# Performance work log

Measured on AMD Instinct MI355X. Metric: run time of the kernel, lower is better.

## Reference

```python
import jax, jax.numpy as jnp
import numpy as np

WS = 8        # window_size
SHIFT = 4     # shift_size
NH = 6        # num_heads
EPS = 1e-5


def _rel_pos_index(ws):
    coords = np.stack(np.meshgrid(np.arange(ws), np.arange(ws), indexing='ij'))  # [2,ws,ws]
    cf = coords.reshape(2, -1)                      # [2, ws*ws]
    rel = cf[:, :, None] - cf[:, None, :]           # [2, N, N]
    rel = rel.transpose(1, 2, 0)                    # [N, N, 2]
    rel[:, :, 0] += ws - 1
    rel[:, :, 1] += ws - 1
    rel[:, :, 0] *= 2 * ws - 1
    return rel.sum(-1)                              # [N, N] int


def _attn_mask(H, W, ws, shift):
    img = np.zeros((H, W), dtype=np.float32)
    slices = (slice(0, -ws), slice(-ws, -shift), slice(-shift, None))
    cnt = 0
    for hs in slices:
        for wsl in slices:
            img[hs, wsl] = cnt
            cnt += 1
    mw = img.reshape(H // ws, ws, W // ws, ws).transpose(0, 2, 1, 3).reshape(-1, ws * ws)
    diff = mw[:, None, :] - mw[:, :, None]          # [nW, N, N]
    return np.where(diff != 0, -100.0, 0.0).astype(np.float32)


def _layernorm(x, g, b):
    mu = x.mean(-1, keepdims=True)
    var = ((x - mu) ** 2).mean(-1, keepdims=True)
    return (x - mu) * jax.lax.rsqrt(var + EPS) * g + b


def setup_inputs() -> dict:
    key = jax.random.key(0)
    ks = jax.random.split(key, 8)
    C, HID = 192, 768
    return {
        'x': jax.random.normal(ks[0], (8, 128, 128, C), jnp.float32),
        'g1': jnp.ones((C,), jnp.float32),
        'b1': jnp.zeros((C,), jnp.float32),
        'qkv_w': jax.random.normal(ks[1], (3 * C, C), jnp.float32) * 0.02,
        'qkv_b': jnp.zeros((3 * C,), jnp.float32),
        'rpb_table': jax.random.normal(ks[2], ((2 * WS - 1) ** 2, NH), jnp.float32) * 0.02,
        'proj_w': jax.random.normal(ks[3], (C, C), jnp.float32) * 0.02,
        'proj_b': jnp.zeros((C,), jnp.float32),
        'g2': jnp.ones((C,), jnp.float32),
        'b2': jnp.zeros((C,), jnp.float32),
        'fc1_w': jax.random.normal(ks[4], (HID, C), jnp.float32) * 0.02,
        'fc1_b': jnp.zeros((HID,), jnp.float32),
        'fc2_w': jax.random.normal(ks[5], (C, HID), jnp.float32) * 0.02,
        'fc2_b': jnp.zeros((C,), jnp.float32),
    }


def reference(x, g1, b1, qkv_w, qkv_b, rpb_table, proj_w, proj_b, g2, b2,
              fc1_w, fc1_b, fc2_w, fc2_b):
    B, H, W, C = x.shape
    N = WS * WS
    hd = C // NH
    scale = hd ** -0.5

    rpi = jnp.asarray(_rel_pos_index(WS))                 # [N,N] static
    mask = jnp.asarray(_attn_mask(H, W, WS, SHIFT))       # [nW,N,N] static
    nW = mask.shape[0]

    shortcut = x.reshape(B, H * W, C)
    xn = _layernorm(shortcut, g1, b1).reshape(B, H, W, C)

    # cyclic shift
    xs = jnp.roll(xn, shift=(-SHIFT, -SHIFT), axis=(1, 2))

    # window partition -> [B*nW, N, C]
    win = xs.reshape(B, H // WS, WS, W // WS, WS, C).transpose(0, 1, 3, 2, 4, 5)
    win = win.reshape(-1, N, C)
    B_ = win.shape[0]

    # qkv
    qkv = jnp.einsum('bnc,oc->bno', win, qkv_w) + qkv_b   # [B_,N,3C]
    qkv = qkv.reshape(B_, N, 3, NH, hd).transpose(2, 0, 3, 1, 4)  # [3,B_,NH,N,hd]
    q, k, v = qkv[0] * scale, qkv[1], qkv[2]

    attn = jnp.einsum('bhnd,bhmd->bhnm', q, k)            # [B_,NH,N,N]
    bias = rpb_table[rpi.reshape(-1)].reshape(N, N, NH).transpose(2, 0, 1)
    attn = attn + bias[None]
    attn = attn.reshape(B, nW, NH, N, N) + mask[None, :, None]
    attn = jax.nn.softmax(attn.reshape(B_, NH, N, N), axis=-1)

    out = jnp.einsum('bhnm,bhmd->bhnd', attn, v)          # [B_,NH,N,hd]
    out = out.transpose(0, 2, 1, 3).reshape(B_, N, C)
    out = jnp.einsum('bnc,oc->bno', out, proj_w) + proj_b

    # window reverse -> [B,H,W,C]
    out = out.reshape(B, H // WS, W // WS, WS, WS, C).transpose(0, 1, 3, 2, 4, 5)
    out = out.reshape(B, H, W, C)
    out = jnp.roll(out, shift=(SHIFT, SHIFT), axis=(1, 2)).reshape(B, H * W, C)

    x1 = shortcut + out
    h = _layernorm(x1, g2, b2)
    h = jnp.einsum('bnc,hc->bnh', h, fc1_w) + fc1_b
    h = jax.nn.gelu(h, approximate=False)
    h = jnp.einsum('bnh,ch->bnc', h, fc2_w) + fc2_b
    x2 = x1 + h
    return x2.reshape(B, H, W, C)
```

## Files before the change

kernel.cpp:

```cpp
#include <hip/hip_runtime.h>
#include <hip/hip_bf16.h>

typedef __attribute__((ext_vector_type(8))) short s16x8;
typedef __attribute__((ext_vector_type(4))) float f32x4;

__device__ __forceinline__ unsigned short f2bf(float f){
    __hip_bfloat16 h = __float2bfloat16(f);
    return *reinterpret_cast<unsigned short*>(&h);
}

__device__ __forceinline__ int flab(int g){ return (g < 120) ? 0 : ((g < 124) ? 1 : 2); }

__device__ __forceinline__ void async16(const void* g, void* l){
    __builtin_amdgcn_global_load_lds(
        (const __attribute__((address_space(1))) unsigned int*)g,
        (__attribute__((address_space(3))) unsigned int*)l, 16, 0, 0);
}

__global__ __launch_bounds__(256) void wconv_all(
    const float* __restrict__ w0, const float* __restrict__ w1,
    const float* __restrict__ w2, const float* __restrict__ w3,
    unsigned short* __restrict__ o0, unsigned short* __restrict__ o1,
    unsigned short* __restrict__ o2, unsigned short* __restrict__ o3)
{
    int i = blockIdx.x*256 + threadIdx.x;
    if (i < 110592) o0[i] = f2bf(w0[i]);
    if (i < 36864)  o1[i] = f2bf(w1[i]);
    if (i < 147456) o2[i] = f2bf(w2[i]);
    if (i < 147456) o3[i] = f2bf(w3[i]);
}

__global__ __launch_bounds__(256) void lnqkv_kernel(
    const float* __restrict__ x, const float* __restrict__ g1, const float* __restrict__ b1,
    const unsigned short* __restrict__ wq, const float* __restrict__ qkvb,
    unsigned short* __restrict__ qo, unsigned short* __restrict__ ko,
    unsigned short* __restrict__ vo)
{
    __shared__ __attribute__((aligned(16))) unsigned short win[64*200];
    __shared__ __attribute__((aligned(16))) unsigned short Bs[64*200];
    const int b_ = blockIdx.x;
    const int bb = b_>>8, wi = b_&255, wh = wi>>4, ww = wi&15;
    const int tid = threadIdx.x;
    const int wv = tid>>6, lane = tid&63, lrow = lane&15, quad = lane>>4;

    {
        const int n = tid>>2, q4 = tid&3;
        const int r = n>>3, c = n&7;
        const int hh = (wh*8 + r + 4)&127, wp = (ww*8 + c + 4)&127;
        const float* px = x + (((size_t)bb*128+hh)*128+wp)*192 + q4*48;
        float v[48];
        #pragma unroll
        for (int m=0;m<12;++m) *(float4*)(v+m*4) = *(const float4*)(px+m*4);
        float s = 0.f;
        #pragma unroll
        for (int k=0;k<48;++k) s += v[k];
        s += __shfl_xor(s,1); s += __shfl_xor(s,2);
        float mu = s*(1.0f/192.0f);
        float qv = 0.f;
        #pragma unroll
        for (int k=0;k<48;++k){ float d=v[k]-mu; qv += d*d; }
        qv += __shfl_xor(qv,1); qv += __shfl_xor(qv,2);
        float rstd = rsqrtf(qv*(1.0f/192.0f) + 1e-5f);
        const float* pg = g1 + q4*48;
        const float* pb = b1 + q4*48;
        unsigned short* pw = win + n*200 + q4*48;
        #pragma unroll
        for (int k=0;k<48;++k) pw[k] = f2bf((v[k]-mu)*rstd*pg[k] + pb[k]);
    }
    __syncthreads();

    s16x8 af[6];
    #pragma unroll
    for (int kc=0;kc<6;++kc)
        af[kc] = *(const s16x8*)(win + (wv*16+lrow)*200 + kc*32 + quad*8);

    for (int ot=0; ot<9; ++ot) {
        const int o0 = ot*64;
        __syncthreads();
        #pragma unroll
        for (int t=0;t<6;++t) {
            int cid = tid + t*256;
            *(int4*)(Bs + (cid/24)*200 + (cid%24)*8) =
                *(const int4*)(wq + (size_t)o0*192 + cid*8);
        }
        __syncthreads();
        f32x4 acc[4];
        #pragma unroll
        for (int j=0;j<4;++j) acc[j] = (f32x4){0.f,0.f,0.f,0.f};
        #pragma unroll
        for (int kc=0;kc<6;++kc)
            #pragma unroll
            for (int j=0;j<4;++j) {
                s16x8 bf = *(const s16x8*)(Bs + (j*16+lrow)*200 + kc*32 + quad*8);
                acc[j] = __builtin_amdgcn_mfma_f32_16x16x32_bf16(af[kc], bf, acc[j], 0, 0, 0);
            }
        __syncthreads();
        unsigned short* T = Bs;
        const int part = ot/3;
        float bv[4];
        #pragma unroll
        for (int j=0;j<4;++j) bv[j] = qkvb[o0 + j*16 + lrow];

        if (part < 2) {
            const float scale = (part==0) ? 0.17677669529663687f : 1.0f;
            #pragma unroll
            for (int j=0;j<4;++j)
                #pragma unroll
                for (int rg=0;rg<4;++rg) {
                    int n2 = wv*16 + quad*4 + rg;
                    T[n2*72 + j*16 + lrow] = f2bf((acc[j][rg]+bv[j])*scale);
                }
            __syncthreads();
            unsigned short* dst = (part==0) ? qo : ko;
            #pragma unroll
            for (int t=0;t<2;++t) {
                int c = tid + t*256;
                int n2 = c>>3, blk = c&7;
                int o_in = o0 + blk*8 - part*192;
                int head = o_in>>5, d = o_in&31;
                *(int4*)(dst + (((size_t)b_*6+head)*64 + n2)*32 + d) =
                    *(const int4*)(T + n2*72 + blk*8);
            }
        } else {
            #pragma unroll
            for (int j=0;j<4;++j)
                #pragma unroll
                for (int rg=0;rg<4;++rg) {
                    int n2 = wv*16 + quad*4 + rg;
                    T[(j*16+lrow)*72 + n2] = f2bf(acc[j][rg]+bv[j]);
                }
            __syncthreads();
            #pragma unroll
            for (int t=0;t<2;++t) {
                int c = tid + t*256;
                int ol = c>>3, nb = (c&7)*8;
                int o_in = o0 + ol - 384;
                int head = o_in>>5, d = o_in&31;
                *(int4*)(vo + (((size_t)b_*6+head)*32 + d)*64 + nb) =
                    *(const int4*)(T + ol*72 + nb);
            }
        }
    }
}

__global__ __launch_bounds__(384) void attn_kernel(
    const unsigned short* __restrict__ q, const unsigned short* __restrict__ k,
    const unsigned short* __restrict__ vT, const float* __restrict__ rpb,
    unsigned short* __restrict__ ao)
{
    __shared__ float rpb_s[1350];
    __shared__ __attribute__((aligned(16))) unsigned short p_lds[6*4608];
    const int b_ = blockIdx.x;
    const int h = threadIdx.x >> 6;
    const int lane = threadIdx.x & 63, lrow = lane & 15, quad = lane >> 4;
    for (int i = threadIdx.x; i < 1350; i += 384) rpb_s[i] = rpb[i];
    __syncthreads();

    const size_t hb = ((size_t)b_*6 + h)*2048;
    const unsigned short* qb = q  + hb;
    const unsigned short* kb = k  + hb;
    const unsigned short* vb = vT + hb;

    s16x8 qf[4], kf[4];
    #pragma unroll
    for (int i = 0; i < 4; ++i) qf[i] = *(const s16x8*)(qb + (i*16+lrow)*32 + quad*8);
    #pragma unroll
    for (int j = 0; j < 4; ++j) kf[j] = *(const s16x8*)(kb + (j*16+lrow)*32 + quad*8);

    const f32x4 zz = {0.f,0.f,0.f,0.f};
    f32x4 s[4][4];
    #pragma unroll
    for (int i = 0; i < 4; ++i)
        #pragma unroll
        for (int j = 0; j < 4; ++j)
            s[i][j] = __builtin_amdgcn_mfma_f32_16x16x32_bf16(qf[i], kf[j], zz, 0, 0, 0);

    const int wi = b_ & 255, wh = wi >> 4, ww = wi & 15;
    int labm[4];
    #pragma unroll
    for (int j = 0; j < 4; ++j) {
        int m = j*16 + lrow;
        labm[j] = flab(wh*8 + (m >> 3))*3 + flab(ww*8 + (m & 7));
    }
    unsigned short* pl = p_lds + h*4608;
    #pragma unroll
    for (int i = 0; i < 4; ++i) {
        #pragma unroll
        for (int rg = 0; rg < 4; ++rg) {
            int n = i*16 + quad*4 + rg;
            int rn = n >> 3, cn = n & 7;
            int labn = flab(wh*8 + rn)*3 + flab(ww*8 + cn);
            float vals[4];
            float vmax = -1e30f;
            #pragma unroll
            for (int j = 0; j < 4; ++j) {
                int m = j*16 + lrow;
                int idx = ((rn - (m >> 3) + 7)*15 + (cn - (m & 7) + 7))*6 + h;
                float val = s[i][j][rg] + rpb_s[idx];
                if (labn != labm[j]) val -= 100.f;
                vals[j] = val;
                vmax = fmaxf(vmax, val);
            }
            #pragma unroll
            for (int o = 1; o < 16; o <<= 1) vmax = fmaxf(vmax, __shfl_xor(vmax, o));
            float sum = 0.f;
            #pragma unroll
            for (int j = 0; j < 4; ++j) { vals[j] = __expf(vals[j] - vmax); sum += vals[j]; }
            #pragma unroll
            for (int o = 1; o < 16; o <<= 1) sum += __shfl_xor(sum, o);
            float inv = 1.f / sum;
            #pragma unroll
            for (int j = 0; j < 4; ++j) pl[n*72 + j*16 + lrow] = f2bf(vals[j]*inv);
        }
    }
    __syncthreads();

    f32x4 oacc[4][2];
    #pragma unroll
    for (int i = 0; i < 4; ++i) { oacc[i][0] = zz; oacc[i][1] = zz; }
    #pragma unroll
    for (int kc = 0; kc < 2; ++kc) {
        s16x8 vf[2];
        #pragma unroll
        for (int jd = 0; jd < 2; ++jd)
            vf[jd] = *(const s16x8*)(vb + (jd*16+lrow)*64 + kc*32 + quad*8);
        #pragma unroll
        for (int i = 0; i < 4; ++i) {
            s16x8 pf = *(const s16x8*)(pl + (i*16+lrow)*72 + kc*32 + quad*8);
            #pragma unroll
            for (int jd = 0; jd < 2; ++jd)
                oacc[i][jd] = __builtin_amdgcn_mfma_f32_16x16x32_bf16(pf, vf[jd], oacc[i][jd], 0, 0, 0);
        }
    }
    unsigned short* ob = ao + (size_t)b_*12288 + h*32;
    #pragma unroll
    for (int i = 0; i < 4; ++i)
        #pragma unroll
        for (int jd = 0; jd < 2; ++jd)
            #pragma unroll
            for (int rg = 0; rg < 4; ++rg) {
                int n = i*16 + quad*4 + rg;
                ob[(size_t)n*192 + jd*16 + lrow] = f2bf(oacc[i][jd][rg]);
            }
}

__global__ __launch_bounds__(256) void projln_kernel(
    const unsigned short* __restrict__ A, const unsigned short* __restrict__ W,
    const float* __restrict__ pbias, const float* __restrict__ x,
    const float* __restrict__ g2, const float* __restrict__ b2,
    float* __restrict__ x1, unsigned short* __restrict__ xln2)
{
    __shared__ __attribute__((aligned(16))) char smem[36864];
    unsigned short* As = (unsigned short*)smem;
    unsigned short* Bs = (unsigned short*)(smem + 9216);
    const int b_ = blockIdx.x;
    const int tid = threadIdx.x, wv = tid>>6, lane = tid&63;
    const int lrow = lane&15, quad = lane>>4;
    const size_t m0 = (size_t)b_*64;

    f32x4 acc[12];
    #pragma unroll
    for (int j=0;j<12;++j) acc[j] = (f32x4){0.f,0.f,0.f,0.f};

    for (int k0=0;k0<192;k0+=64) {
        __syncthreads();
        #pragma unroll
        for (int t=0;t<2;++t) {
            int cid = tid + t*256;
            *(int4*)(As + (cid>>3)*72 + (cid&7)*8) =
                *(const int4*)(A + (m0 + (cid>>3))*192 + k0 + (cid&7)*8);
        }
        #pragma unroll
        for (int t=0;t<6;++t) {
            int cid = tid + t*256;
            *(int4*)(Bs + (cid>>3)*72 + (cid&7)*8) =
                *(const int4*)(W + (size_t)(cid>>3)*192 + k0 + (cid&7)*8);
        }
        __syncthreads();
        #pragma unroll
        for (int kc=0;kc<2;++kc) {
            s16x8 af = *(const s16x8*)(As + (wv*16+lrow)*72 + kc*32 + quad*8);
            #pragma unroll
            for (int j=0;j<12;++j) {
                s16x8 bf = *(const s16x8*)(Bs + (j*16+lrow)*72 + kc*32 + quad*8);
                acc[j] = __builtin_amdgcn_mfma_f32_16x16x32_bf16(af, bf, acc[j], 0, 0, 0);
            }
        }
    }
    __syncthreads();

    const int bb = b_>>8, wi = b_&255, wh = wi>>4, ww = wi&15;
    float bv[12], gv[12], b2v[12];
    #pragma unroll
    for (int j=0;j<12;++j) {
        bv[j]  = pbias[j*16+lrow];
        gv[j]  = g2[j*16+lrow];
        b2v[j] = b2[j*16+lrow];
    }
    unsigned short* T = (unsigned short*)smem;
    #pragma unroll
    for (int rg=0;rg<4;++rg) {
        int n2 = wv*16 + quad*4 + rg;
        int r = n2>>3, c = n2&7;
        int hh = (wh*8+r+4)&127, wp = (ww*8+c+4)&127;
        size_t tok = ((size_t)bb*128+hh)*128 + wp;
        float xv[12];
        float s = 0.f;
        #pragma unroll
        for (int j=0;j<12;++j) {
            float t = acc[j][rg] + bv[j] + x[tok*192 + j*16 + lrow];
            xv[j] = t; s += t;
        }
        #pragma unroll
        for (int o=1;o<16;o<<=1) s += __shfl_xor(s, o);
        float mu = s*(1.0f/192.0f);
        float qv = 0.f;
        #pragma unroll
        for (int j=0;j<12;++j){ float d = xv[j]-mu; qv += d*d; }
        #pragma unroll
        for (int o=1;o<16;o<<=1) qv += __shfl_xor(qv, o);
        float rstd = rsqrtf(qv*(1.0f/192.0f) + 1e-5f);
        #pragma unroll
        for (int j=0;j<12;++j) {
            x1[tok*192 + j*16 + lrow] = xv[j];
            T[n2*200 + j*16 + lrow] = f2bf((xv[j]-mu)*rstd*gv[j] + b2v[j]);
        }
    }
    __syncthreads();
    #pragma unroll
    for (int t=0;t<6;++t) {
        int cid = tid + t*256;
        int n2 = cid/24, blk = cid%24;
        int r = n2>>3, c = n2&7;
        int hh = (wh*8+r+4)&127, wp = (ww*8+c+4)&127;
        size_t tok = ((size_t)bb*128+hh)*128 + wp;
        *(int4*)(xln2 + tok*192 + blk*8) = *(const int4*)(T + n2*200 + blk*8);
    }
}

template<int K>
__device__ __forceinline__ void mm128x96(
    const unsigned short* __restrict__ A, const unsigned short* __restrict__ W,
    size_t m0, int o0, unsigned short* As, unsigned short* Bs,
    f32x4 (&acc)[2][6])
{
    const int tid = threadIdx.x, wv = tid>>6, lane = tid&63;
    const int lrow = lane&15, quad = lane>>4;
    const int grow = lane>>2;
    const int gcb  = (lane&3) ^ ((lane>>3)&3);
    #pragma unroll
    for (int i=0;i<2;++i)
        #pragma unroll
        for (int j=0;j<6;++j) acc[i][j] = (f32x4){0.f,0.f,0.f,0.f};

    const unsigned short* Ab = A + (m0 + grow)*(size_t)K + gcb*8;
    const unsigned short* Wb = W + ((size_t)(o0 + grow))*K + gcb*8;

    auto issue = [&](int k0, int buf) {
        unsigned short* Ad = As + buf*4096;
        unsigned short* Bd = Bs + buf*3072;
        async16(Ab + (size_t)(wv*16)*K + k0,     Ad + wv*512);
        async16(Ab + (size_t)((wv+4)*16)*K + k0, Ad + (wv+4)*512);
        async16(Wb + (size_t)(wv*16)*K + k0,     Bd + wv*512);
        if (wv < 2)
            async16(Wb + (size_t)((wv+4)*16)*K + k0, Bd + (wv+4)*512);
    };
    auto compute = [&](int buf) {
        const unsigned short* Ac = As + buf*4096;
        const unsigned short* Bc = Bs + buf*3072;
        const int rs = (quad ^ ((lrow>>1)&3)) << 3;
        s16x8 af[2], bf[6];
        #pragma unroll
        for (int i=0;i<2;++i)
            af[i] = *(const s16x8*)(Ac + (wv*32 + i*16 + lrow)*32 + rs);
        #pragma unroll
        for (int j=0;j<6;++j)
            bf[j] = *(const s16x8*)(Bc + (j*16 + lrow)*32 + rs);
        #pragma unroll
        for (int i=0;i<2;++i)
            #pragma unroll
            for (int j=0;j<6;++j)
                acc[i][j] = __builtin_amdgcn_mfma_f32_16x16x32_bf16(af[i], bf[j], acc[i][j], 0, 0, 0);
    };

    constexpr int NT = K/32;
    issue(0, 0);
    issue(32, 1);
    int cur = 0;
    for (int t = 0; t < NT-2; ++t) {
        if (wv < 2) asm volatile("s_waitcnt vmcnt(4)" ::: "memory");
        else        asm volatile("s_waitcnt vmcnt(3)" ::: "memory");
        __builtin_amdgcn_s_barrier();
        asm volatile("" ::: "memory");
        int nb = cur + 2; if (nb >= 3) nb -= 3;
        issue((t+2)*32, nb);
        asm volatile("" ::: "memory");
        compute(cur);
        cur = (cur == 2) ? 0 : cur + 1;
    }
    if (wv < 2) asm volatile("s_waitcnt vmcnt(4)" ::: "memory");
    else        asm volatile("s_waitcnt vmcnt(3)" ::: "memory");
    __builtin_amdgcn_s_barrier();
    asm volatile("" ::: "memory");
    compute(cur);
    cur = (cur == 2) ? 0 : cur + 1;
    asm volatile("s_waitcnt vmcnt(0)" ::: "memory");
    __builtin_amdgcn_s_barrier();
    asm volatile("" ::: "memory");
    compute(cur);
}

__global__ __launch_bounds__(256, 3) void gemm_fc1_kernel(
    const unsigned short* __restrict__ A, const unsigned short* __restrict__ Wm,
    const float* __restrict__ bias, unsigned short* __restrict__ h1)
{
    __shared__ __attribute__((aligned(16))) char smem[43008];
    unsigned short* As = (unsigned short*)smem;
    unsigned short* Bs = (unsigned short*)(smem + 24576);
    const int bid = blockIdx.x;
    const int virt = (bid & 7)*1024 + (bid >> 3);
    const size_t m0 = (size_t)(virt >> 3)*128;
    const int o0 = (virt & 7)*96;
    f32x4 acc[2][6];
    mm128x96<192>(A, Wm, m0, o0, As, Bs, acc);
    const int tid = threadIdx.x, wv = tid>>6, lane = tid&63;
    const int lrow = lane&15, quad = lane>>4;
    float bv[6];
    #pragma unroll
    for (int j=0;j<6;++j) bv[j] = bias[o0 + j*16 + lrow];
    __syncthreads();
    unsigned short* T = (unsigned short*)smem;
    #pragma unroll
    for (int i=0;i<2;++i)
        #pragma unroll
        for (int j=0;j<6;++j)
            #pragma unroll
            for (int rg=0;rg<4;++rg) {
                int ml = wv*32 + i*16 + quad*4 + rg;
                float v = acc[i][j][rg] + bv[j];
                float v2 = v*v;
                float z = v*(1.5957691216057308f + 0.07135481627f*v2);
                float r = v * __builtin_amdgcn_rcpf(1.f + __expf(-z));
                T[ml*104 + j*16 + lrow] = f2bf(r);
            }
    __syncthreads();
    #pragma unroll
    for (int t=0;t<6;++t) {
        int c = tid + t*256;
        int row = c/12, blk = c%12;
        *(int4*)(h1 + (m0+row)*768 + o0 + blk*8) = *(const int4*)(T + row*104 + blk*8);
    }
}

__global__ __launch_bounds__(256, 3) void gemm_fc2_kernel(
    const unsigned short* __restrict__ A, const unsigned short* __restrict__ Wm,
    const float* __restrict__ bias, const float* __restrict__ x1, float* __restrict__ out)
{
    __shared__ __attribute__((aligned(16))) char smem[43008];
    unsigned short* As = (unsigned short*)smem;
    unsigned short* Bs = (unsigned short*)(smem + 24576);
    const int bid = blockIdx.x;
    const int virt = (bid & 7)*256 + (bid >> 3);
    const size_t m0 = (size_t)(virt >> 1)*128;
    const int o0 = (virt & 1)*96;
    f32x4 acc[2][6];
    mm128x96<768>(A, Wm, m0, o0, As, Bs, acc);
    const int tid = threadIdx.x, wv = tid>>6, lane = tid&63;
    const int lrow = lane&15, quad = lane>>4;
    float bv[6];
    #pragma unroll
    for (int j=0;j<6;++j) bv[j] = bias[o0 + j*16 + lrow];
    float* T = (float*)smem;
    #pragma unroll
    for (int p=0;p<2;++p) {
        __syncthreads();
        if ((wv>>1) == p) {
            int wl = wv&1;
            #pragma unroll
            for (int i=0;i<2;++i)
                #pragma unroll
                for (int j=0;j<6;++j)
                    #pragma unroll
                    for (int rg=0;rg<4;++rg)
                        T[(wl*32 + i*16 + quad*4 + rg)*100 + j*16 + lrow] = acc[i][j][rg] + bv[j];
        }
        __syncthreads();
        #pragma unroll
        for (int t=0;t<6;++t) {
            int c = tid + t*256;
            int row = c/24, blk = c%24;
            size_t ad = (m0 + p*64 + row)*192 + o0 + blk*4;
            float4 v = *(const float4*)(T + row*100 + blk*4);
            float4 rx = *(const float4*)(x1 + ad);
            v.x += rx.x; v.y += rx.y; v.z += rx.z; v.w += rx.w;
            *(float4*)(out + ad) = v;
        }
    }
}

extern "C" void kernel_launch(void* const* d_in, const int* in_sizes, int n_in,
                              void* d_out, int out_size, void* d_ws, size_t ws_size,
                              hipStream_t stream)
{
    const float* x      = (const float*)d_in[0];
    const float* g1     = (const float*)d_in[1];
    const float* b1     = (const float*)d_in[2];
    const float* qkv_w  = (const float*)d_in[3];
    const float* qkv_b  = (const float*)d_in[4];
    const float* rpb    = (const float*)d_in[5];
    const float* proj_w = (const float*)d_in[6];
    const float* proj_b = (const float*)d_in[7];
    const float* g2     = (const float*)d_in[8];
    const float* b2     = (const float*)d_in[9];
    const float* fc1_w  = (const float*)d_in[10];
    const float* fc1_b  = (const float*)d_in[11];
    const float* fc2_w  = (const float*)d_in[12];
    const float* fc2_b  = (const float*)d_in[13];
    float* out = (float*)d_out;
    char* ws = (char*)d_ws;

    if (ws_size < 353206272ULL) return;

    unsigned short* qbuf  = (unsigned short*)(ws + 0);
    unsigned short* kbuf  = (unsigned short*)(ws + 50331648);
    unsigned short* vbuf  = (unsigned short*)(ws + 100663296);
    unsigned short* attnO = (unsigned short*)(ws + 150994944);
    float*          x1    = (float*)        (ws + 201326592);
    unsigned short* xln2  = (unsigned short*)(ws + 301989888);
    unsigned short* wq    = (unsigned short*)(ws + 352321536);
    unsigned short* wp    = (unsigned short*)(ws + 352321536 + 221184);
    unsigned short* w1    = (unsigned short*)(ws + 352321536 + 221184 + 73728);
    unsigned short* w2    = (unsigned short*)(ws + 352321536 + 221184 + 73728 + 294912);
    unsigned short* h1    = (unsigned short*)(ws + 0);

    wconv_all<<<576, 256, 0, stream>>>(qkv_w, proj_w, fc1_w, fc2_w, wq, wp, w1, w2);
    lnqkv_kernel<<<2048, 256, 0, stream>>>(x, g1, b1, wq, qkv_b, qbuf, kbuf, vbuf);
    attn_kernel<<<2048, 384, 0, stream>>>(qbuf, kbuf, vbuf, rpb, attnO);
    projln_kernel<<<2048, 256, 0, stream>>>(attnO, wp, proj_b, x, g2, b2, x1, xln2);
    gemm_fc1_kernel<<<8192, 256, 0, stream>>>(xln2, w1, fc1_b, h1);
    gemm_fc2_kernel<<<2048, 256, 0, stream>>>(h1, w2, fc2_b, x1, out);
}
```

Baseline: 579.4 us.

## Simplify GEMM pipelines to double-buffered async LDS loads and raise occupancy

Result: faster. 564.3 us (-2.6%).

```diff
diff --git a/kernel.cpp b/kernel.cpp
--- a/kernel.cpp
+++ b/kernel.cpp
@@ -244,49 +244,60 @@
             }
 }
 
+__device__ __forceinline__ void mm64x192(
+    const unsigned short* __restrict__ A, const unsigned short* __restrict__ W,
+    size_t m0, unsigned short* As, unsigned short* Bs, f32x4 (&acc)[12])
+{
+    const int tid = threadIdx.x, wv = tid>>6, lane = tid&63;
+    const int lrow = lane&15, quad = lane>>4;
+    const int grow = lane>>2;
+    const int gcb  = (lane&3) ^ ((lane>>3)&3);
+    #pragma unroll
+    for (int j=0;j<12;++j) acc[j] = (f32x4){0.f,0.f,0.f,0.f};
+
+    const unsigned short* Ab = A + (m0 + grow)*192 + gcb*8;
+    const unsigned short* Wb = W + (size_t)grow*192 + gcb*8;
+
+    auto issue = [&](int k0, unsigned short* Ad, unsigned short* Bd) {
+        async16(Ab + (size_t)(wv*16)*192 + k0,     Ad + wv*512);
+        async16(Wb + (size_t)(wv*16)*192 + k0,     Bd + wv*512);
+        async16(Wb + (size_t)((wv+4)*16)*192 + k0, Bd + (wv+4)*512);
+        async16(Wb + (size_t)((wv+8)*16)*192 + k0, Bd + (wv+8)*512);
+    };
+    issue(0, As, Bs);
+    int cur = 0;
+    for (int k0=0; k0<192; k0+=32) {
+        __syncthreads();
+        if (k0+32 < 192) issue(k0+32, As + (cur^1)*2048, Bs + (cur^1)*6144);
+        const unsigned short* Ac = As + cur*2048;
+        const unsigned short* Bc = Bs + cur*6144;
+        const int rs = (quad ^ ((lrow>>1)&3)) << 3;
+        s16x8 af = *(const s16x8*)(Ac + (wv*16+lrow)*32 + rs);
+        #pragma unroll
+        for (int j=0;j<12;++j) {
+            s16x8 bf = *(const s16x8*)(Bc + (j*16+lrow)*32 + rs);
+            acc[j] = __builtin_amdgcn_mfma_f32_16x16x32_bf16(af, bf, acc[j], 0, 0, 0);
+        }
+        cur ^= 1;
+    }
+}
+
 __global__ __launch_bounds__(256) void projln_kernel(
     const unsigned short* __restrict__ A, const unsigned short* __restrict__ W,
     const float* __restrict__ pbias, const float* __restrict__ x,
     const float* __restrict__ g2, const float* __restrict__ b2,
     float* __restrict__ x1, unsigned short* __restrict__ xln2)
 {
-    __shared__ __attribute__((aligned(16))) char smem[36864];
+    __shared__ __attribute__((aligned(16))) char smem[32768];
     unsigned short* As = (unsigned short*)smem;
-    unsigned short* Bs = (unsigned short*)(smem + 9216);
+    unsigned short* Bs = (unsigned short*)(smem + 8192);
     const int b_ = blockIdx.x;
     const int tid = threadIdx.x, wv = tid>>6, lane = tid&63;
     const int lrow = lane&15, quad = lane>>4;
     const size_t m0 = (size_t)b_*64;
 
     f32x4 acc[12];
-    #pragma unroll
-    for (int j=0;j<12;++j) acc[j] = (f32x4){0.f,0.f,0.f,0.f};
-
-    for (int k0=0;k0<192;k0+=64) {
-        __syncthreads();
-        #pragma unroll
-        for (int t=0;t<2;++t) {
-            int cid = tid + t*256;
-            *(int4*)(As + (cid>>3)*72 + (cid&7)*8) =
-                *(const int4*)(A + (m0 + (cid>>3))*192 + k0 + (cid&7)*8);
-        }
-        #pragma unroll
-        for (int t=0;t<6;++t) {
-            int cid = tid + t*256;
-            *(int4*)(Bs + (cid>>3)*72 + (cid&7)*8) =
-                *(const int4*)(W + (size_t)(cid>>3)*192 + k0 + (cid&7)*8);
-        }
-        __syncthreads();
-        #pragma unroll
-        for (int kc=0;kc<2;++kc) {
-            s16x8 af = *(const s16x8*)(As + (wv*16+lrow)*72 + kc*32 + quad*8);
-            #pragma unroll
-            for (int j=0;j<12;++j) {
-                s16x8 bf = *(const s16x8*)(Bs + (j*16+lrow)*72 + kc*32 + quad*8);
-                acc[j] = __builtin_amdgcn_mfma_f32_16x16x32_bf16(af, bf, acc[j], 0, 0, 0);
-            }
-        }
-    }
+    mm64x192(A, W, m0, As, Bs, acc);
     __syncthreads();
 
     const int bb = b_>>8, wi = b_&255, wh = wi>>4, ww = wi&15;
@@ -356,18 +367,20 @@
     const unsigned short* Ab = A + (m0 + grow)*(size_t)K + gcb*8;
     const unsigned short* Wb = W + ((size_t)(o0 + grow))*K + gcb*8;
 
-    auto issue = [&](int k0, int buf) {
-        unsigned short* Ad = As + buf*4096;
-        unsigned short* Bd = Bs + buf*3072;
+    auto issue = [&](int k0, unsigned short* Ad, unsigned short* Bd) {
         async16(Ab + (size_t)(wv*16)*K + k0,     Ad + wv*512);
         async16(Ab + (size_t)((wv+4)*16)*K + k0, Ad + (wv+4)*512);
         async16(Wb + (size_t)(wv*16)*K + k0,     Bd + wv*512);
         if (wv < 2)
             async16(Wb + (size_t)((wv+4)*16)*K + k0, Bd + (wv+4)*512);
     };
-    auto compute = [&](int buf) {
-        const unsigned short* Ac = As + buf*4096;
-        const unsigned short* Bc = Bs + buf*3072;
+    issue(0, As, Bs);
+    int cur = 0;
+    for (int k0=0; k0<K; k0+=32) {
+        __syncthreads();
+        if (k0+32 < K) issue(k0+32, As + (cur^1)*4096, Bs + (cur^1)*3072);
+        const unsigned short* Ac = As + cur*4096;
+        const unsigned short* Bc = Bs + cur*3072;
         const int rs = (quad ^ ((lrow>>1)&3)) << 3;
         s16x8 af[2], bf[6];
         #pragma unroll
@@ -381,42 +394,17 @@
             #pragma unroll
             for (int j=0;j<6;++j)
                 acc[i][j] = __builtin_amdgcn_mfma_f32_16x16x32_bf16(af[i], bf[j], acc[i][j], 0, 0, 0);
-    };
-
-    constexpr int NT = K/32;
-    issue(0, 0);
-    issue(32, 1);
-    int cur = 0;
-    for (int t = 0; t < NT-2; ++t) {
-        if (wv < 2) asm volatile("s_waitcnt vmcnt(4)" ::: "memory");
-        else        asm volatile("s_waitcnt vmcnt(3)" ::: "memory");
-        __builtin_amdgcn_s_barrier();
-        asm volatile("" ::: "memory");
-        int nb = cur + 2; if (nb >= 3) nb -= 3;
-        issue((t+2)*32, nb);
-        asm volatile("" ::: "memory");
-        compute(cur);
-        cur = (cur == 2) ? 0 : cur + 1;
-    }
-    if (wv < 2) asm volatile("s_waitcnt vmcnt(4)" ::: "memory");
-    else        asm volatile("s_waitcnt vmcnt(3)" ::: "memory");
-    __builtin_amdgcn_s_barrier();
-    asm volatile("" ::: "memory");
-    compute(cur);
-    cur = (cur == 2) ? 0 : cur + 1;
-    asm volatile("s_waitcnt vmcnt(0)" ::: "memory");
-    __builtin_amdgcn_s_barrier();
-    asm volatile("" ::: "memory");
-    compute(cur);
-}
-
-__global__ __launch_bounds__(256, 3) void gemm_fc1_kernel(
+        cur ^= 1;
+    }
+}
+
+__global__ __launch_bounds__(256, 4) void gemm_fc1_kernel(
     const unsigned short* __restrict__ A, const unsigned short* __restrict__ Wm,
     const float* __restrict__ bias, unsigned short* __restrict__ h1)
 {
-    __shared__ __attribute__((aligned(16))) char smem[43008];
+    __shared__ __attribute__((aligned(16))) char smem[28672];
     unsigned short* As = (unsigned short*)smem;
-    unsigned short* Bs = (unsigned short*)(smem + 24576);
+    unsigned short* Bs = (unsigned short*)(smem + 16384);
     const int bid = blockIdx.x;
     const int virt = (bid & 7)*1024 + (bid >> 3);
     const size_t m0 = (size_t)(virt >> 3)*128;
@@ -452,13 +440,13 @@
     }
 }
 
-__global__ __launch_bounds__(256, 3) void gemm_fc2_kernel(
+__global__ __launch_bounds__(256, 4) void gemm_fc2_kernel(
     const unsigned short* __restrict__ A, const unsigned short* __restrict__ Wm,
     const float* __restrict__ bias, const float* __restrict__ x1, float* __restrict__ out)
 {
-    __shared__ __attribute__((aligned(16))) char smem[43008];
+    __shared__ __attribute__((aligned(16))) char smem[28672];
     unsigned short* As = (unsigned short*)smem;
-    unsigned short* Bs = (unsigned short*)(smem + 24576);
+    unsigned short* Bs = (unsigned short*)(smem + 16384);
     const int bid = blockIdx.x;
     const int virt = (bid & 7)*256 + (bid >> 3);
     const size_t m0 = (size_t)(virt >> 1)*128;
```
